# Optimization experiments

Measured on AMD Instinct MI355X. Metric: run time of the kernel, lower is better.

Reference implementation:

```python
import jax, jax.numpy as jnp
import numpy as np


def setup_inputs() -> dict:
    key = jax.random.key(0)
    ks = jax.random.split(key, 8)
    B, C, H, W = 4, 256, 64, 64
    Cqk = C // 8
    s = 0.05
    return {
        "x": jax.random.normal(ks[0], (B, C, H, W), jnp.float32),
        "Wq": jax.random.normal(ks[1], (Cqk, C), jnp.float32) * s,
        "bq": jax.random.normal(ks[2], (Cqk,), jnp.float32) * s,
        "Wk": jax.random.normal(ks[3], (Cqk, C), jnp.float32) * s,
        "bk": jax.random.normal(ks[4], (Cqk,), jnp.float32) * s,
        "Wv": jax.random.normal(ks[5], (C, C), jnp.float32) * s,
        "bv": jax.random.normal(ks[6], (C,), jnp.float32) * s,
        "gamma": jax.random.normal(ks[7], (1,), jnp.float32),
    }


def reference(x, Wq, bq, Wk, bk, Wv, bv, gamma):
    B, C, H, W = x.shape
    N = H * W
    xf = x.reshape(B, C, N)                      # [B,C,N]
    # 1x1 convs == channel matmuls
    q = jnp.einsum('oc,bcn->bon', Wq, xf) + bq[None, :, None]   # [B,C/8,N]
    k = jnp.einsum('oc,bcn->bon', Wk, xf) + bk[None, :, None]   # [B,C/8,N]
    v = jnp.einsum('oc,bcn->bon', Wv, xf) + bv[None, :, None]   # [B,C,N]
    # scores[b,i,j] = <q[:,i], k[:,j]>; softmax over j (last dim)
    scores = jnp.einsum('bci,bcj->bij', q, k)                   # [B,N,N]
    attn = jax.nn.softmax(scores, axis=-1)
    # out[b,c,i] = sum_j v[b,c,j] * attn[b,i,j]
    out = jnp.einsum('bcj,bij->bci', v, attn).reshape(B, C, H, W)
    return gamma[0] * out + x
```

## Files before the change

### kernel.cpp

```cpp
#include <hip/hip_runtime.h>


#define B_ 4
#define C_ 256
#define N_ 4096
#define CQK 32

typedef __attribute__((ext_vector_type(8))) short short8;
typedef __attribute__((ext_vector_type(4))) short short4v;
typedef __attribute__((ext_vector_type(16))) float f32x16;
typedef __attribute__((ext_vector_type(4))) float f32x4;

__device__ __forceinline__ unsigned short f2bf(float f) {
  unsigned int u = __builtin_bit_cast(unsigned int, f);
  u = (u + 0x7fffu + ((u >> 16) & 1u)) >> 16;
  return (unsigned short)u;
}
__device__ __forceinline__ float bf2f(unsigned short s) {
  unsigned int u = ((unsigned int)s) << 16;
  return __builtin_bit_cast(float, u);
}
__device__ __forceinline__ f32x16 mfma16(short8 a, short8 b, f32x16 c) {
  return __builtin_amdgcn_mfma_f32_32x32x16_bf16(a, b, c, 0, 0, 0);
}
__device__ __forceinline__ int swz64(int row, int col) {
  return row * 64 + ((((col >> 3) ^ row) & 7) << 3) + (col & 7);
}
__device__ __forceinline__ int swz32(int row, int col) {
  return row * 32 + ((((col >> 3) ^ row) & 3) << 3) + (col & 7);
}

#define GL16(gp, lp)                                                     \
  __builtin_amdgcn_global_load_lds(                                      \
      (const __attribute__((address_space(1))) unsigned int*)(gp),       \
      (__attribute__((address_space(3))) unsigned int*)(lp), 16, 0, 0)

#define WAITCNT(s) asm volatile("s_waitcnt " s ::: "memory")
#define BARRIER()                         \
  do {                                    \
    __builtin_amdgcn_s_barrier();         \
    asm volatile("" ::: "memory");        \
  } while (0)

__global__ __launch_bounds__(256) void k_prep(
    const float* __restrict__ x, unsigned short* __restrict__ xthi,
    unsigned short* __restrict__ xtlo,
    const float* __restrict__ Wq, const float* __restrict__ Wk,
    const float* __restrict__ Wv,
    unsigned short* __restrict__ wqh, unsigned short* __restrict__ wql,
    unsigned short* __restrict__ wkh, unsigned short* __restrict__ wkl,
    unsigned short* __restrict__ wvh, unsigned short* __restrict__ wvl) {
  __shared__ __align__(16) float tile[64 * 65];
  const int bi = blockIdx.x;
  const int t = threadIdx.x;
  if (bi < 1024) {
    const int it = bi & 63, ct = (bi >> 6) & 3, b = bi >> 8;
    const int i0 = it * 64, c0 = ct * 64;
    {
      const int i = t & 63, cb = t >> 6;
#pragma unroll
      for (int z = 0; z < 16; ++z) {
        const int c = z * 4 + cb;
        tile[i * 65 + c] = x[(b * C_ + c0 + c) * N_ + i0 + i];
      }
    }
    __syncthreads();
    {
      const int ii = t >> 2, p = t & 3;
      short8 h0, h1, l0, l1;
#pragma unroll
      for (int e = 0; e < 16; ++e) {
        const float f = tile[ii * 65 + p * 16 + e];
        const unsigned short hb = f2bf(f);
        const unsigned short lb = f2bf(f - bf2f(hb));
        if (e < 8) { h0[e] = (short)hb; l0[e] = (short)lb; }
        else       { h1[e - 8] = (short)hb; l1[e - 8] = (short)lb; }
      }
      const int base = (b * N_ + i0 + ii) * C_ + c0 + p * 16;
      *(short8*)(xthi + base) = h0;
      *(short8*)(xthi + base + 8) = h1;
      *(short8*)(xtlo + base) = l0;
      *(short8*)(xtlo + base + 8) = l1;
    }
  } else {
    const int e = (bi - 1024) * 256 + t;
    const float* src; unsigned short *hi, *lo; int idx;
    if (e < 8192)        { src = Wq; hi = wqh; lo = wql; idx = e; }
    else if (e < 16384)  { src = Wk; hi = wkh; lo = wkl; idx = e - 8192; }
    else                 { src = Wv; hi = wvh; lo = wvl; idx = e - 16384; }
    const float f = src[idx];
    const unsigned short h = f2bf(f);
    hi[idx] = h;
    lo[idx] = f2bf(f - bf2f(h));
  }
}

__global__ __launch_bounds__(256) void k_proj(
    const unsigned short* __restrict__ wqh, const unsigned short* __restrict__ wql,
    const unsigned short* __restrict__ wkh, const unsigned short* __restrict__ wkl,
    const unsigned short* __restrict__ wvh, const unsigned short* __restrict__ wvl,
    const unsigned short* __restrict__ xthi, const unsigned short* __restrict__ xtlo,
    const float* __restrict__ bq, const float* __restrict__ bk,
    const float* __restrict__ bv,
    unsigned short* __restrict__ qhg, unsigned short* __restrict__ qlg,
    unsigned short* __restrict__ khg, unsigned short* __restrict__ klg,
    unsigned short* __restrict__ vg) {
  __shared__ __align__(16) char sm[33792];
  unsigned short* awh = (unsigned short*)sm;
  unsigned short* awl = awh + 4096;
  unsigned short* bxh = awl + 4096;
  unsigned short* bxl = bxh + 4096;
  float* qt = (float*)sm;

  const int it = blockIdx.x, ot = blockIdx.y, b = blockIdx.z;
  const int i0 = it * 64, o0 = ot * 64;
  const int t = threadIdx.x, lane = t & 63, w = t >> 6, h = lane >> 5;
  const int mb = w >> 1, nb = w & 1;
  const int srow = t >> 2, sp = t & 3;

  const int og = o0 + srow;
  const unsigned short *wh, *wl;
  if (og < 32)      { wh = wqh + og * C_;        wl = wql + og * C_; }
  else if (og < 64) { wh = wkh + (og - 32) * C_; wl = wkl + (og - 32) * C_; }
  else              { wh = wvh + (og - 64) * C_; wl = wvl + (og - 64) * C_; }
  const unsigned short* xh = xthi + (b * N_ + i0 + srow) * C_;
  const unsigned short* xl = xtlo + (b * N_ + i0 + srow) * C_;

  f32x16 acc;
#pragma unroll
  for (int e = 0; e < 16; ++e) acc[e] = 0.f;
  const int m = 32 * mb + (lane & 31);
  const int n = 32 * nb + (lane & 31);

  for (int kt = 0; kt < 4; ++kt) {
    const int cb = kt * 64 + sp * 16;
    *(short8*)&awh[swz64(srow, sp * 16)]     = *(const short8*)(wh + cb);
    *(short8*)&awh[swz64(srow, sp * 16 + 8)] = *(const short8*)(wh + cb + 8);
    *(short8*)&awl[swz64(srow, sp * 16)]     = *(const short8*)(wl + cb);
    *(short8*)&awl[swz64(srow, sp * 16 + 8)] = *(const short8*)(wl + cb + 8);
    *(short8*)&bxh[swz64(srow, sp * 16)]     = *(const short8*)(xh + cb);
    *(short8*)&bxh[swz64(srow, sp * 16 + 8)] = *(const short8*)(xh + cb + 8);
    *(short8*)&bxl[swz64(srow, sp * 16)]     = *(const short8*)(xl + cb);
    *(short8*)&bxl[swz64(srow, sp * 16 + 8)] = *(const short8*)(xl + cb + 8);
    __syncthreads();
#pragma unroll
    for (int kk = 0; kk < 4; ++kk) {
      const int kb = kk * 16 + h * 8;
      const short8 ah  = *(const short8*)&awh[swz64(m, kb)];
      const short8 al2 = *(const short8*)&awl[swz64(m, kb)];
      const short8 bh  = *(const short8*)&bxh[swz64(n, kb)];
      const short8 bl2 = *(const short8*)&bxl[swz64(n, kb)];
      acc = mfma16(ah, bh, acc);
      acc = mfma16(ah, bl2, acc);
      acc = mfma16(al2, bh, acc);
    }
    __syncthreads();
  }

  if (ot > 0) {
#pragma unroll
    for (int e = 0; e < 16; ++e) {
      const int r = 32 * mb + (e & 3) + 8 * (e >> 2) + 4 * h;
      const int oc = o0 - 64 + r;
      vg[(b * C_ + oc) * N_ + i0 + n] = f2bf(acc[e] + bv[oc]);
    }
  } else {
#pragma unroll
    for (int e = 0; e < 16; ++e) {
      const int r = 32 * mb + (e & 3) + 8 * (e >> 2) + 4 * h;
      const float bias = (r < 32) ? bq[r] : bk[r - 32];
      qt[r * 65 + n] = acc[e] + bias;
    }
    __syncthreads();
    const int ii = t >> 2;
    short8 hv0, hv1, lv0, lv1;
#pragma unroll
    for (int e = 0; e < 16; ++e) {
      const float f = qt[(sp * 16 + e) * 65 + ii];
      const unsigned short hb = f2bf(f);
      const unsigned short lb = f2bf(f - bf2f(hb));
      if (e < 8) { hv0[e] = (short)hb; lv0[e] = (short)lb; }
      else       { hv1[e - 8] = (short)hb; lv1[e - 8] = (short)lb; }
    }
    if (sp < 2) {
      const int base = (b * N_ + i0 + ii) * CQK + sp * 16;
      *(short8*)(qhg + base) = hv0; *(short8*)(qhg + base + 8) = hv1;
      *(short8*)(qlg + base) = lv0; *(short8*)(qlg + base + 8) = lv1;
    } else {
      const int base = (b * N_ + i0 + ii) * CQK + sp * 16 - 32;
      *(short8*)(khg + base) = hv0; *(short8*)(khg + base + 8) = hv1;
      *(short8*)(klg + base) = lv0; *(short8*)(klg + base + 8) = lv1;
    }
  }
}

__global__ __launch_bounds__(512, 4) void k_flash(
    const unsigned short* __restrict__ qhg, const unsigned short* __restrict__ qlg,
    const unsigned short* __restrict__ khg, const unsigned short* __restrict__ klg,
    const unsigned short* __restrict__ vg,
    unsigned short* __restrict__ Opart, float* __restrict__ mlpart) {
  __shared__ __align__(16) char sm[65536];
  float* stf = (float*)sm;
  char* stb = sm;
  unsigned short* kh = (unsigned short*)(sm + 16384);
  unsigned short* kl = (unsigned short*)(sm + 20480);
  unsigned short* vt = (unsigned short*)(sm + 24576);
  float* alphaf = (float*)(sm + 57344);
  float* otf = (float*)sm;

  const int blk = blockIdx.x;
  const int b = (blk >> 1) & 3;
  const int half = blk & 1;
  const int qt_ = blk >> 3;
  const int q0 = qt_ * 64;
  const int jbase = half * 2048;
  const int t = threadIdx.x, lane = t & 63, w = t >> 6, h = lane >> 5;
  const int l31 = lane & 31;
  const int r_sm = t >> 3, p_sm = t & 7;
  const int mbs = (w >> 1) & 1, nbs = w & 1;

  const int krow = 16 * (w & 3) + (lane >> 2);
  const int kg = (lane & 3) ^ (krow & 3);
  const unsigned short* kgsrc = ((w < 4) ? khg : klg) +
      (size_t)(b * N_ + jbase + krow) * CQK + kg * 8;
  unsigned short* kldst = ((w < 4) ? kh : kl) + (w & 3) * 512;
  const int vc = 32 * w + (lane >> 3);
  const int vgg = (lane & 7) ^ ((lane >> 3) & 7);
  const unsigned short* vgsrc =
      vg + (size_t)(b * C_ + vc) * N_ + jbase + vgg * 8;
  unsigned short* vldst = vt + 32 * w * 64;

  GL16(kgsrc, kldst);
#pragma unroll
  for (int q = 0; q < 4; ++q)
    GL16(vgsrc + q * 8 * N_, vldst + q * 8 * 64);

  short8 qfh[2], qfl[2];
  {
    const unsigned short* qph =
        qhg + (size_t)(b * N_ + q0 + 32 * mbs + l31) * CQK + h * 8;
    const unsigned short* qpl =
        qlg + (size_t)(b * N_ + q0 + 32 * mbs + l31) * CQK + h * 8;
    if (w < 4) {
#pragma unroll
      for (int kk = 0; kk < 2; ++kk) {
        qfh[kk] = *(const short8*)(qph + kk * 16);
        qfl[kk] = *(const short8*)(qpl + kk * 16);
      }
    }
  }

  f32x16 acc0, acc1;
#pragma unroll
  for (int e = 0; e < 16; ++e) { acc0[e] = 0.f; acc1[e] = 0.f; }
  float m_run = -1e30f, l_run = 0.f;

  for (int kt = 0; kt < 32; ++kt) {
    WAITCNT("vmcnt(4) lgkmcnt(0)");
    BARRIER();
    if (w < 4) {
      f32x16 sa;
#pragma unroll
      for (int e = 0; e < 16; ++e) sa[e] = 0.f;
      const int jn = 32 * nbs + l31;
      __builtin_amdgcn_s_setprio(1);
#pragma unroll
      for (int kk = 0; kk < 2; ++kk) {
        const short8 bh = *(const short8*)&kh[swz32(jn, kk * 16 + h * 8)];
        const short8 bl = *(const short8*)&kl[swz32(jn, kk * 16 + h * 8)];
        sa = mfma16(qfh[kk], bh, sa);
        sa = mfma16(qfh[kk], bl, sa);
        sa = mfma16(qfl[kk], bh, sa);
      }
      __builtin_amdgcn_s_setprio(0);
#pragma unroll
      for (int e = 0; e < 16; ++e) {
        const int ri = 32 * mbs + (e & 3) + 8 * (e >> 2) + 4 * h;
        stf[ri * 64 + ((((jn >> 2) ^ ri) & 15) << 2) + (jn & 3)] = sa[e];
      }
    }
    WAITCNT("lgkmcnt(0)");
    BARRIER();
    {
      const int ktn = (kt + 1 < 32) ? kt + 1 : 31;
      GL16(kgsrc + ktn * 64 * CQK, kldst);
    }
    {
      float* p0 = stf + r_sm * 64 + ((((2 * p_sm) ^ r_sm) & 15) << 2);
      float* p1 = stf + r_sm * 64 + ((((2 * p_sm + 1) ^ r_sm) & 15) << 2);
      const f32x4 a0 = *(const f32x4*)p0;
      const f32x4 a1 = *(const f32x4*)p1;
      float s[8];
#pragma unroll
      for (int e = 0; e < 4; ++e) { s[e] = a0[e]; s[4 + e] = a1[e]; }
      float mx = s[0];
#pragma unroll
      for (int e = 1; e < 8; ++e) mx = fmaxf(mx, s[e]);
      mx = fmaxf(mx, __shfl_xor(mx, 1));
      mx = fmaxf(mx, __shfl_xor(mx, 2));
      mx = fmaxf(mx, __shfl_xor(mx, 4));
      const float mnew = fmaxf(m_run, mx);
      const float al = __expf(m_run - mnew);
      float ts = 0.f;
      short8 pv8;
#pragma unroll
      for (int e = 0; e < 8; ++e) {
        const float pe = __expf(s[e] - mnew);
        ts += pe;
        pv8[e] = (short)f2bf(pe);
      }
      ts += __shfl_xor(ts, 1);
      ts += __shfl_xor(ts, 2);
      ts += __shfl_xor(ts, 4);
      l_run = l_run * al + ts;
      m_run = mnew;
      *(short8*)p0 = pv8;
      if (p_sm == 0) alphaf[r_sm] = al;
    }
    WAITCNT("lgkmcnt(0)");
    BARRIER();
#pragma unroll
    for (int eq = 0; eq < 4; ++eq) {
      const f32x4 av0 = *(const f32x4*)&alphaf[4 * h + 8 * eq];
      const f32x4 av1 = *(const f32x4*)&alphaf[32 + 4 * h + 8 * eq];
#pragma unroll
      for (int q = 0; q < 4; ++q) {
        acc0[4 * eq + q] *= av0[q];
        acc1[4 * eq + q] *= av1[q];
      }
    }
    WAITCNT("vmcnt(1)");
    {
      const int crow = 32 * w + l31;
      __builtin_amdgcn_s_setprio(1);
#pragma unroll
      for (int kk = 0; kk < 4; ++kk) {
        const int g0 = ((4 * kk + 2 * h) ^ l31) & 15;
        const short8 pa0 = *(const short8*)(stb + l31 * 256 + (g0 << 4));
        const short8 pa1 = *(const short8*)(stb + (32 + l31) * 256 + (g0 << 4));
        const short8 vf = *(const short8*)&vt[swz64(crow, kk * 16 + h * 8)];
        acc0 = mfma16(pa0, vf, acc0);
        acc1 = mfma16(pa1, vf, acc1);
      }
      __builtin_amdgcn_s_setprio(0);
    }
    WAITCNT("lgkmcnt(0)");
    {
      const int ktv = (kt + 1 < 32) ? kt + 1 : 31;
      const unsigned short* vs = vgsrc + ktv * 64;
#pragma unroll
      for (int q = 0; q < 4; ++q)
        GL16(vs + q * 8 * N_, vldst + q * 8 * 64);
    }
  }

  if (p_sm == 0) {
    mlpart[blk * 128 + r_sm] = m_run;
    mlpart[blk * 128 + 64 + r_sm] = l_run;
  }
  WAITCNT("vmcnt(0) lgkmcnt(0)");
  BARRIER();
  {
    const int cc = 32 * w + l31;
#pragma unroll
    for (int e = 0; e < 16; ++e) {
      const int r0 = (e & 3) + 8 * (e >> 2) + 4 * h;
      otf[cc * 64 + ((((r0 >> 2) ^ cc) & 15) << 2) + (r0 & 3)] = acc0[e];
      const int r1 = 32 + r0;
      otf[cc * 64 + ((((r1 >> 2) ^ cc) & 15) << 2) + (r1 & 3)] = acc1[e];
    }
  }
  WAITCNT("lgkmcnt(0)");
  BARRIER();
#pragma unroll
  for (int pass = 0; pass < 8; ++pass) {
    const int idx = pass * 512 + t;
    const int c = idx >> 4, gi = idx & 15;
    const f32x4 ov = *(const f32x4*)(otf + c * 64 + (((gi ^ c) & 15) << 2));
    short4v hv;
#pragma unroll
    for (int q = 0; q < 4; ++q) {
      const _Float16 hf = (_Float16)ov[q];
      hv[q] = __builtin_bit_cast(short, hf);
    }
    *(short4v*)(Opart + blk * 16384 + c * 64 + gi * 4) = hv;
  }
}

__global__ __launch_bounds__(256) void k_combine(
    const unsigned short* __restrict__ Opart, const float* __restrict__ mlpart,
    const float* __restrict__ x, const float* __restrict__ gamma,
    float* __restrict__ out) {
  const int cb = blockIdx.x;
  const int b = cb & 3, qt_ = cb >> 2;
  const int q0 = qt_ * 64;
  const int blk1 = (qt_ << 3) | (b << 1);
  const int blk2 = blk1 | 1;
  const int t = threadIdx.x;
  const int i = t & 63, cg = t >> 6;

  const float m1 = mlpart[blk1 * 128 + i], l1 = mlpart[blk1 * 128 + 64 + i];
  const float m2 = mlpart[blk2 * 128 + i], l2 = mlpart[blk2 * 128 + 64 + i];
  const float M = fmaxf(m1, m2);
  const float w1 = __expf(m1 - M), w2 = __expf(m2 - M);
  const float inv = 1.f / (w1 * l1 + w2 * l2);
  const float gm = gamma[0];
  const float s1 = gm * w1 * inv, s2 = gm * w2 * inv;

  const unsigned short* p1 = Opart + blk1 * 16384 + i;
  const unsigned short* p2 = Opart + blk2 * 16384 + i;
#pragma unroll 4
  for (int c = cg; c < C_; c += 4) {
    const float o1 = (float)__builtin_bit_cast(_Float16, p1[c * 64]);
    const float o2 = (float)__builtin_bit_cast(_Float16, p2[c * 64]);
    const int g = (b * C_ + c) * N_ + q0 + i;
    out[g] = s1 * o1 + s2 * o2 + x[g];
  }
}

extern "C" void kernel_launch(void* const* d_in, const int* in_sizes, int n_in,
                              void* d_out, int out_size, void* d_ws, size_t ws_size,
                              hipStream_t stream) {
  const float* x     = (const float*)d_in[0];
  const float* Wq    = (const float*)d_in[1];
  const float* bq    = (const float*)d_in[2];
  const float* Wk    = (const float*)d_in[3];
  const float* bk    = (const float*)d_in[4];
  const float* Wv    = (const float*)d_in[5];
  const float* bv    = (const float*)d_in[6];
  const float* gamma = (const float*)d_in[7];
  float* out = (float*)d_out;
  (void)in_sizes; (void)n_in; (void)out_size; (void)ws_size;

  char* ws = (char*)d_ws;
  size_t off = 0;
  auto carve = [&](size_t bytes) -> char* {
    char* p = ws + off;
    off += (bytes + 255) & ~(size_t)255;
    return p;
  };
  unsigned short* xthi = (unsigned short*)carve((size_t)B_ * N_ * C_ * 2);
  unsigned short* xtlo = (unsigned short*)carve((size_t)B_ * N_ * C_ * 2);
  unsigned short* wqh  = (unsigned short*)carve(32 * 256 * 2);
  unsigned short* wql  = (unsigned short*)carve(32 * 256 * 2);
  unsigned short* wkh  = (unsigned short*)carve(32 * 256 * 2);
  unsigned short* wkl  = (unsigned short*)carve(32 * 256 * 2);
  unsigned short* wvh  = (unsigned short*)carve(256 * 256 * 2);
  unsigned short* wvl  = (unsigned short*)carve(256 * 256 * 2);
  unsigned short* qhg  = (unsigned short*)carve((size_t)B_ * N_ * CQK * 2);
  unsigned short* qlg  = (unsigned short*)carve((size_t)B_ * N_ * CQK * 2);
  unsigned short* khg  = (unsigned short*)carve((size_t)B_ * N_ * CQK * 2);
  unsigned short* klg  = (unsigned short*)carve((size_t)B_ * N_ * CQK * 2);
  unsigned short* vg   = (unsigned short*)carve((size_t)B_ * C_ * N_ * 2);
  unsigned short* Opart = (unsigned short*)carve((size_t)512 * 16384 * 2);
  float* mlpart = (float*)carve((size_t)512 * 128 * 4);

  k_prep<<<1344, 256, 0, stream>>>(x, xthi, xtlo, Wq, Wk, Wv,
                                   wqh, wql, wkh, wkl, wvh, wvl);
  k_proj<<<dim3(64, 5, B_), 256, 0, stream>>>(wqh, wql, wkh, wkl, wvh, wvl,
                                              xthi, xtlo, bq, bk, bv,
                                              qhg, qlg, khg, klg, vg);
  k_flash<<<512, 512, 0, stream>>>(qhg, qlg, khg, klg, vg, Opart, mlpart);
  k_combine<<<256, 256, 0, stream>>>(Opart, mlpart, x, gamma, out);
}
```

Measured before the change: 200.2 us.

## Warp-specialize flash kernel into score producers and PV consumers with double-buffered P

```diff
diff --git a/kernel.cpp b/kernel.cpp
--- a/kernel.cpp
+++ b/kernel.cpp
@@ -20,20 +20,16 @@
   unsigned int u = ((unsigned int)s) << 16;
   return __builtin_bit_cast(float, u);
 }
+__device__ __forceinline__ short f32tof16(float f) {
+  const _Float16 hf = (_Float16)f;
+  return __builtin_bit_cast(short, hf);
+}
 __device__ __forceinline__ f32x16 mfma16(short8 a, short8 b, f32x16 c) {
   return __builtin_amdgcn_mfma_f32_32x32x16_bf16(a, b, c, 0, 0, 0);
 }
 __device__ __forceinline__ int swz64(int row, int col) {
   return row * 64 + ((((col >> 3) ^ row) & 7) << 3) + (col & 7);
 }
-__device__ __forceinline__ int swz32(int row, int col) {
-  return row * 32 + ((((col >> 3) ^ row) & 3) << 3) + (col & 7);
-}
-
-#define GL16(gp, lp)                                                     \
-  __builtin_amdgcn_global_load_lds(                                      \
-      (const __attribute__((address_space(1))) unsigned int*)(gp),       \
-      (__attribute__((address_space(3))) unsigned int*)(lp), 16, 0, 0)
 
 #define WAITCNT(s) asm volatile("s_waitcnt " s ::: "memory")
 #define BARRIER()                         \
@@ -194,19 +190,16 @@
   }
 }
 
-__global__ __launch_bounds__(512, 4) void k_flash(
+__global__ __launch_bounds__(768, 3) void k_flash(
     const unsigned short* __restrict__ qhg, const unsigned short* __restrict__ qlg,
     const unsigned short* __restrict__ khg, const unsigned short* __restrict__ klg,
     const unsigned short* __restrict__ vg,
     unsigned short* __restrict__ Opart, float* __restrict__ mlpart) {
-  __shared__ __align__(16) char sm[65536];
-  float* stf = (float*)sm;
-  char* stb = sm;
-  unsigned short* kh = (unsigned short*)(sm + 16384);
-  unsigned short* kl = (unsigned short*)(sm + 20480);
-  unsigned short* vt = (unsigned short*)(sm + 24576);
-  float* alphaf = (float*)(sm + 57344);
-  float* otf = (float*)sm;
+  __shared__ __align__(16) char sm[17920];
+  char* Pb0 = sm;
+  char* Pb1 = sm + 8192;
+  float* alphaA = (float*)(sm + 16384);
+  float* mlm = (float*)(sm + 16896);
 
   const int blk = blockIdx.x;
   const int b = (blk >> 1) & 3;
@@ -216,174 +209,171 @@
   const int jbase = half * 2048;
   const int t = threadIdx.x, lane = t & 63, w = t >> 6, h = lane >> 5;
   const int l31 = lane & 31;
-  const int r_sm = t >> 3, p_sm = t & 7;
-  const int mbs = (w >> 1) & 1, nbs = w & 1;
-
-  const int krow = 16 * (w & 3) + (lane >> 2);
-  const int kg = (lane & 3) ^ (krow & 3);
-  const unsigned short* kgsrc = ((w < 4) ? khg : klg) +
-      (size_t)(b * N_ + jbase + krow) * CQK + kg * 8;
-  unsigned short* kldst = ((w < 4) ? kh : kl) + (w & 3) * 512;
-  const int vc = 32 * w + (lane >> 3);
-  const int vgg = (lane & 7) ^ ((lane >> 3) & 7);
-  const unsigned short* vgsrc =
-      vg + (size_t)(b * C_ + vc) * N_ + jbase + vgg * 8;
-  unsigned short* vldst = vt + 32 * w * 64;
-
-  GL16(kgsrc, kldst);
-#pragma unroll
-  for (int q = 0; q < 4; ++q)
-    GL16(vgsrc + q * 8 * N_, vldst + q * 8 * 64);
-
-  short8 qfh[2], qfl[2];
-  {
-    const unsigned short* qph =
-        qhg + (size_t)(b * N_ + q0 + 32 * mbs + l31) * CQK + h * 8;
-    const unsigned short* qpl =
-        qlg + (size_t)(b * N_ + q0 + 32 * mbs + l31) * CQK + h * 8;
-    if (w < 4) {
+
+  if (w < 8) {
+    const int c = 32 * w + l31;
+    const unsigned short* vsrc = vg + (size_t)(b * C_ + c) * N_ + jbase + h * 8;
+    f32x16 acc0, acc1;
+#pragma unroll
+    for (int e = 0; e < 16; ++e) { acc0[e] = 0.f; acc1[e] = 0.f; }
+    short8 vf[4];
+#pragma unroll
+    for (int kk = 0; kk < 4; ++kk)
+      vf[kk] = *(const short8*)(vsrc + kk * 16);
+    WAITCNT("lgkmcnt(0)");
+    BARRIER();
+
+#pragma unroll 2
+    for (int kt = 0; kt < 32; ++kt) {
+      const char* pb = (kt & 1) ? Pb1 : Pb0;
+      const float* alp = alphaA + (kt & 1) * 64;
+#pragma unroll
+      for (int eq = 0; eq < 4; ++eq) {
+        const f32x4 av0 = *(const f32x4*)(alp + 8 * eq + 4 * h);
+        const f32x4 av1 = *(const f32x4*)(alp + 32 + 8 * eq + 4 * h);
+#pragma unroll
+        for (int q = 0; q < 4; ++q) {
+          acc0[4 * eq + q] *= av0[q];
+          acc1[4 * eq + q] *= av1[q];
+        }
+      }
+      __builtin_amdgcn_s_setprio(1);
+#pragma unroll
+      for (int kk = 0; kk < 4; ++kk) {
+        const int phys = (2 * kk + h) ^ (l31 & 7);
+        const short8 pa0 = *(const short8*)(pb + l31 * 128 + phys * 16);
+        const short8 pa1 = *(const short8*)(pb + (32 + l31) * 128 + phys * 16);
+        acc0 = mfma16(pa0, vf[kk], acc0);
+        acc1 = mfma16(pa1, vf[kk], acc1);
+      }
+      __builtin_amdgcn_s_setprio(0);
+      if (kt + 1 < 32) {
+#pragma unroll
+        for (int kk = 0; kk < 4; ++kk)
+          vf[kk] = *(const short8*)(vsrc + (kt + 1) * 64 + kk * 16);
+      }
+      WAITCNT("lgkmcnt(0)");
+      BARRIER();
+    }
+    {
+      unsigned short* dst = Opart + (size_t)blk * 16384 + (w * 64 + lane) * 32;
+      short8 o0, o1, o2, o3;
+#pragma unroll
+      for (int e = 0; e < 8; ++e) {
+        o0[e] = f32tof16(acc0[e]);
+        o1[e] = f32tof16(acc0[8 + e]);
+        o2[e] = f32tof16(acc1[e]);
+        o3[e] = f32tof16(acc1[8 + e]);
+      }
+      *(short8*)(dst) = o0;
+      *(short8*)(dst + 8) = o1;
+      *(short8*)(dst + 16) = o2;
+      *(short8*)(dst + 24) = o3;
+    }
+  } else {
+    const int sw = w - 8;
+    const int pair = sw >> 1;
+    const int rb = sw & 1;
+    const int srow = rb * 32 + l31;
+    short8 qfh[2], qfl[2];
+    {
+      const unsigned short* qph = qhg + (size_t)(b * N_ + q0 + srow) * CQK + h * 8;
+      const unsigned short* qpl = qlg + (size_t)(b * N_ + q0 + srow) * CQK + h * 8;
 #pragma unroll
       for (int kk = 0; kk < 2; ++kk) {
         qfh[kk] = *(const short8*)(qph + kk * 16);
         qfl[kk] = *(const short8*)(qpl + kk * 16);
       }
     }
-  }
-
-  f32x16 acc0, acc1;
-#pragma unroll
-  for (int e = 0; e < 16; ++e) { acc0[e] = 0.f; acc1[e] = 0.f; }
-  float m_run = -1e30f, l_run = 0.f;
-
-  for (int kt = 0; kt < 32; ++kt) {
-    WAITCNT("vmcnt(4) lgkmcnt(0)");
-    BARRIER();
-    if (w < 4) {
-      f32x16 sa;
-#pragma unroll
-      for (int e = 0; e < 16; ++e) sa[e] = 0.f;
-      const int jn = 32 * nbs + l31;
+    const unsigned short* kph = khg + (size_t)(b * N_ + jbase + l31) * CQK + h * 8;
+    const unsigned short* kpl = klg + (size_t)(b * N_ + jbase + l31) * CQK + h * 8;
+    short8 kfh[2][2], kfl[2][2];
+    float m_run = -1e30f, l_run = 0.f;
+
+    auto loadK = [&](int tau) {
+#pragma unroll
+      for (int jt = 0; jt < 2; ++jt)
+#pragma unroll
+        for (int kk = 0; kk < 2; ++kk) {
+          kfh[jt][kk] = *(const short8*)(kph + tau * 2048 + jt * 1024 + kk * 16);
+          kfl[jt][kk] = *(const short8*)(kpl + tau * 2048 + jt * 1024 + kk * 16);
+        }
+    };
+    auto s_step = [&](int tau) {
+      f32x16 s0, s1;
+#pragma unroll
+      for (int e = 0; e < 16; ++e) { s0[e] = 0.f; s1[e] = 0.f; }
       __builtin_amdgcn_s_setprio(1);
 #pragma unroll
       for (int kk = 0; kk < 2; ++kk) {
-        const short8 bh = *(const short8*)&kh[swz32(jn, kk * 16 + h * 8)];
-        const short8 bl = *(const short8*)&kl[swz32(jn, kk * 16 + h * 8)];
-        sa = mfma16(qfh[kk], bh, sa);
-        sa = mfma16(qfh[kk], bl, sa);
-        sa = mfma16(qfl[kk], bh, sa);
+        s0 = mfma16(kfh[0][kk], qfh[kk], s0);
+        s0 = mfma16(kfh[0][kk], qfl[kk], s0);
+        s0 = mfma16(kfl[0][kk], qfh[kk], s0);
+        s1 = mfma16(kfh[1][kk], qfh[kk], s1);
+        s1 = mfma16(kfh[1][kk], qfl[kk], s1);
+        s1 = mfma16(kfl[1][kk], qfh[kk], s1);
       }
       __builtin_amdgcn_s_setprio(0);
-#pragma unroll
-      for (int e = 0; e < 16; ++e) {
-        const int ri = 32 * mbs + (e & 3) + 8 * (e >> 2) + 4 * h;
-        stf[ri * 64 + ((((jn >> 2) ^ ri) & 15) << 2) + (jn & 3)] = sa[e];
-      }
-    }
+      if (tau + 2 < 32) loadK(tau + 2);
+      float mprev, lprev;
+      if (tau == 0) { mprev = -1e30f; lprev = 0.f; }
+      else {
+        mprev = mlm[((tau + 1) & 1) * 128 + srow];
+        lprev = mlm[((tau + 1) & 1) * 128 + 64 + srow];
+      }
+      float mx = s0[0];
+#pragma unroll
+      for (int e = 1; e < 16; ++e) mx = fmaxf(mx, s0[e]);
+#pragma unroll
+      for (int e = 0; e < 16; ++e) mx = fmaxf(mx, s1[e]);
+      mx = fmaxf(mx, __shfl_xor(mx, 32));
+      const float mnew = fmaxf(mprev, mx);
+      const float al = __expf(mprev - mnew);
+      float ts = 0.f;
+#pragma unroll
+      for (int e = 0; e < 16; ++e) { s0[e] = __expf(s0[e] - mnew); ts += s0[e]; }
+#pragma unroll
+      for (int e = 0; e < 16; ++e) { s1[e] = __expf(s1[e] - mnew); ts += s1[e]; }
+      ts += __shfl_xor(ts, 32);
+      const float lnew = lprev * al + ts;
+      m_run = mnew;
+      l_run = lnew;
+      char* Pw = (tau & 1) ? Pb1 : Pb0;
+#pragma unroll
+      for (int q = 0; q < 4; ++q) {
+        short4v p0, p1;
+        p0[0] = (short)f2bf(s0[4 * q]);     p0[1] = (short)f2bf(s0[4 * q + 1]);
+        p0[2] = (short)f2bf(s0[4 * q + 2]); p0[3] = (short)f2bf(s0[4 * q + 3]);
+        p1[0] = (short)f2bf(s1[4 * q]);     p1[1] = (short)f2bf(s1[4 * q + 1]);
+        p1[2] = (short)f2bf(s1[4 * q + 2]); p1[3] = (short)f2bf(s1[4 * q + 3]);
+        const int ph0 = q ^ (srow & 7);
+        const int ph1 = (4 + q) ^ (srow & 7);
+        *(short4v*)(Pw + srow * 128 + ph0 * 16 + 8 * h) = p0;
+        *(short4v*)(Pw + srow * 128 + ph1 * 16 + 8 * h) = p1;
+      }
+      if (h == 0) {
+        alphaA[(tau & 1) * 64 + srow] = al;
+        mlm[(tau & 1) * 128 + srow] = mnew;
+        mlm[(tau & 1) * 128 + 64 + srow] = lnew;
+      }
+    };
+
+    loadK(pair);
+    if (pair == 0) s_step(0);
     WAITCNT("lgkmcnt(0)");
     BARRIER();
-    {
-      const int ktn = (kt + 1 < 32) ? kt + 1 : 31;
-      GL16(kgsrc + ktn * 64 * CQK, kldst);
-    }
-    {
-      float* p0 = stf + r_sm * 64 + ((((2 * p_sm) ^ r_sm) & 15) << 2);
-      float* p1 = stf + r_sm * 64 + ((((2 * p_sm + 1) ^ r_sm) & 15) << 2);
-      const f32x4 a0 = *(const f32x4*)p0;
-      const f32x4 a1 = *(const f32x4*)p1;
-      float s[8];
-#pragma unroll
-      for (int e = 0; e < 4; ++e) { s[e] = a0[e]; s[4 + e] = a1[e]; }
-      float mx = s[0];
-#pragma unroll
-      for (int e = 1; e < 8; ++e) mx = fmaxf(mx, s[e]);
-      mx = fmaxf(mx, __shfl_xor(mx, 1));
-      mx = fmaxf(mx, __shfl_xor(mx, 2));
-      mx = fmaxf(mx, __shfl_xor(mx, 4));
-      const float mnew = fmaxf(m_run, mx);
-      const float al = __expf(m_run - mnew);
-      float ts = 0.f;
-      short8 pv8;
-#pragma unroll
-      for (int e = 0; e < 8; ++e) {
-        const float pe = __expf(s[e] - mnew);
-        ts += pe;
-        pv8[e] = (short)f2bf(pe);
-      }
-      ts += __shfl_xor(ts, 1);
-      ts += __shfl_xor(ts, 2);
-      ts += __shfl_xor(ts, 4);
-      l_run = l_run * al + ts;
-      m_run = mnew;
-      *(short8*)p0 = pv8;
-      if (p_sm == 0) alphaf[r_sm] = al;
-    }
-    WAITCNT("lgkmcnt(0)");
-    BARRIER();
-#pragma unroll
-    for (int eq = 0; eq < 4; ++eq) {
-      const f32x4 av0 = *(const f32x4*)&alphaf[4 * h + 8 * eq];
-      const f32x4 av1 = *(const f32x4*)&alphaf[32 + 4 * h + 8 * eq];
-#pragma unroll
-      for (int q = 0; q < 4; ++q) {
-        acc0[4 * eq + q] *= av0[q];
-        acc1[4 * eq + q] *= av1[q];
-      }
-    }
-    WAITCNT("vmcnt(1)");
-    {
-      const int crow = 32 * w + l31;
-      __builtin_amdgcn_s_setprio(1);
-#pragma unroll
-      for (int kk = 0; kk < 4; ++kk) {
-        const int g0 = ((4 * kk + 2 * h) ^ l31) & 15;
-        const short8 pa0 = *(const short8*)(stb + l31 * 256 + (g0 << 4));
-        const short8 pa1 = *(const short8*)(stb + (32 + l31) * 256 + (g0 << 4));
-        const short8 vf = *(const short8*)&vt[swz64(crow, kk * 16 + h * 8)];
-        acc0 = mfma16(pa0, vf, acc0);
-        acc1 = mfma16(pa1, vf, acc1);
-      }
-      __builtin_amdgcn_s_setprio(0);
-    }
-    WAITCNT("lgkmcnt(0)");
-    {
-      const int ktv = (kt + 1 < 32) ? kt + 1 : 31;
-      const unsigned short* vs = vgsrc + ktv * 64;
-#pragma unroll
-      for (int q = 0; q < 4; ++q)
-        GL16(vs + q * 8 * N_, vldst + q * 8 * 64);
-    }
-  }
-
-  if (p_sm == 0) {
-    mlpart[blk * 128 + r_sm] = m_run;
-    mlpart[blk * 128 + 64 + r_sm] = l_run;
-  }
-  WAITCNT("vmcnt(0) lgkmcnt(0)");
-  BARRIER();
-  {
-    const int cc = 32 * w + l31;
-#pragma unroll
-    for (int e = 0; e < 16; ++e) {
-      const int r0 = (e & 3) + 8 * (e >> 2) + 4 * h;
-      otf[cc * 64 + ((((r0 >> 2) ^ cc) & 15) << 2) + (r0 & 3)] = acc0[e];
-      const int r1 = 32 + r0;
-      otf[cc * 64 + ((((r1 >> 2) ^ cc) & 15) << 2) + (r1 & 3)] = acc1[e];
-    }
-  }
-  WAITCNT("lgkmcnt(0)");
-  BARRIER();
-#pragma unroll
-  for (int pass = 0; pass < 8; ++pass) {
-    const int idx = pass * 512 + t;
-    const int c = idx >> 4, gi = idx & 15;
-    const f32x4 ov = *(const f32x4*)(otf + c * 64 + (((gi ^ c) & 15) << 2));
-    short4v hv;
-#pragma unroll
-    for (int q = 0; q < 4; ++q) {
-      const _Float16 hf = (_Float16)ov[q];
-      hv[q] = __builtin_bit_cast(short, hf);
-    }
-    *(short4v*)(Opart + blk * 16384 + c * 64 + gi * 4) = hv;
+
+#pragma unroll 2
+    for (int kt = 0; kt < 32; ++kt) {
+      const int tau = kt + 1;
+      if (tau < 32 && (tau & 1) == pair) s_step(tau);
+      WAITCNT("lgkmcnt(0)");
+      BARRIER();
+    }
+    if (pair == 1 && h == 0) {
+      mlpart[blk * 128 + srow] = m_run;
+      mlpart[blk * 128 + 64 + srow] = l_run;
+    }
   }
 }
 
@@ -407,12 +397,15 @@
   const float gm = gamma[0];
   const float s1 = gm * w1 * inv, s2 = gm * w2 * inv;
 
-  const unsigned short* p1 = Opart + blk1 * 16384 + i;
-  const unsigned short* p2 = Opart + blk2 * 16384 + i;
+  const int hh = (i >> 2) & 1;
+  const int s = ((i >> 5) << 4) + (((i & 31) >> 3) << 2) + (i & 3);
+  const unsigned short* p1 = Opart + (size_t)blk1 * 16384 + hh * 1024 + s;
+  const unsigned short* p2 = Opart + (size_t)blk2 * 16384 + hh * 1024 + s;
 #pragma unroll 4
   for (int c = cg; c < C_; c += 4) {
-    const float o1 = (float)__builtin_bit_cast(_Float16, p1[c * 64]);
-    const float o2 = (float)__builtin_bit_cast(_Float16, p2[c * 64]);
+    const int lb = (c >> 5) * 2048 + (c & 31) * 32;
+    const float o1 = (float)__builtin_bit_cast(_Float16, p1[lb]);
+    const float o2 = (float)__builtin_bit_cast(_Float16, p2[lb]);
     const int g = (b * C_ + c) * N_ + q0 + i;
     out[g] = s1 * o1 + s2 * o2 + x[g];
   }
@@ -460,6 +453,6 @@
   k_proj<<<dim3(64, 5, B_), 256, 0, stream>>>(wqh, wql, wkh, wkl, wvh, wvl,
                                               xthi, xtlo, bq, bk, bv,
                                               qhg, qlg, khg, klg, vg);
-  k_flash<<<512, 512, 0, stream>>>(qhg, qlg, khg, klg, vg, Opart, mlpart);
+  k_flash<<<512, 768, 0, stream>>>(qhg, qlg, khg, klg, vg, Opart, mlpart);
   k_combine<<<256, 256, 0, stream>>>(Opart, mlpart, x, gamma, out);
 }
```

Result: faster. 188.5 us (-5.9%).
